# Optimization experiments

Measured on AMD Instinct MI355X. Metric: run time of the kernel, lower is better.

## Reference

```python
import jax, jax.numpy as jnp
import numpy as np


def _block_triu_mask(seq_len, rows_per_block, cols_per_block, dtype=jnp.float32):
    # Block upper-triangular mask: block (i, j) is ones iff j >= i.
    tri = jnp.triu(jnp.ones((seq_len, seq_len), dtype=dtype))
    return jnp.kron(tri, jnp.ones((rows_per_block, cols_per_block), dtype=dtype))


def setup_inputs() -> dict:
    key = jax.random.key(0)
    k_x, k_w1, k_w2 = jax.random.split(key, 3)
    seq_len, input_dim, hidden_dim, output_dim = 64, 64, 128, 64
    batch = 256
    x = jax.random.normal(k_x, (batch, seq_len, input_dim), dtype=jnp.float32)
    # kaiming_uniform_(a=sqrt(5)) on [fan_in, fan_out] tensor -> bound = 1/sqrt(fan_in)
    fan1 = seq_len * input_dim
    W1 = jax.random.uniform(k_w1, (seq_len * input_dim, seq_len * hidden_dim),
                            minval=-1.0, maxval=1.0, dtype=jnp.float32) / np.sqrt(fan1)
    b1 = jnp.zeros((seq_len * hidden_dim,), dtype=jnp.float32)
    fan2 = seq_len * hidden_dim
    W2 = jax.random.uniform(k_w2, (seq_len * hidden_dim, seq_len * output_dim),
                            minval=-1.0, maxval=1.0, dtype=jnp.float32) / np.sqrt(fan2)
    b2 = jnp.zeros((seq_len * output_dim,), dtype=jnp.float32)
    return {"x": x, "W1": W1, "b1": b1, "W2": W2, "b2": b2, "seq_len": seq_len}


def reference(x, W1, b1, W2, b2, seq_len):
    batch = x.shape[0]
    input_dim = x.shape[2]
    hidden_dim = W1.shape[1] // seq_len
    output_dim = W2.shape[1] // seq_len
    mask1 = _block_triu_mask(seq_len, input_dim, hidden_dim, W1.dtype)
    mask2 = _block_triu_mask(seq_len, hidden_dim, output_dim, W2.dtype)
    h = x.reshape(batch, seq_len * input_dim)
    h = jnp.matmul(h, W1 * mask1) + b1           # [B, S*H]
    h = jax.nn.relu(h)
    h = jnp.matmul(h, W2 * mask2) + b2           # [B, S*O]
    return h.reshape(batch, seq_len, output_dim)
```

## Files before the change

kernel.cpp:

```cpp
#include <hip/hip_runtime.h>

typedef short bf16x8 __attribute__((ext_vector_type(8)));
typedef float f32x4 __attribute__((ext_vector_type(4)));

__device__ __forceinline__ unsigned short f2bf(float f) {
  unsigned x = __float_as_uint(f);
  return (unsigned short)((x + 0x7fffu + ((x >> 16) & 1u)) >> 16);
}

__global__ __launch_bounds__(256)
void init_bias(const float* __restrict__ b, float* __restrict__ out) {
  int i = (blockIdx.x * 256 + threadIdx.x) * 4;
  *(float4*)(out + i) = *(const float4*)(b + (i & 4095));
}

__global__ __launch_bounds__(256)
void bias_relu_inplace(float* __restrict__ h, const float* __restrict__ b) {
  int i = (blockIdx.x * 256 + threadIdx.x) * 4;
  float4 v = *(const float4*)(h + i);
  float4 bv = *(const float4*)(b + (i & 8191));
  v.x = fmaxf(v.x + bv.x, 0.f);
  v.y = fmaxf(v.y + bv.y, 0.f);
  v.z = fmaxf(v.z + bv.z, 0.f);
  v.w = fmaxf(v.w + bv.w, 0.f);
  *(float4*)(h + i) = v;
}

template<int KROW, int CW, int KS>
__global__ __launch_bounds__(256, 3)
void gemm_sk(const float* __restrict__ A, const float* __restrict__ W,
             float* __restrict__ out, int K, int N)
{
  __shared__ unsigned short Xs[128 * 72];
  __shared__ unsigned short Ws[64 * 72];

  const int n0 = blockIdx.x * 64;
  const int m0 = blockIdx.y * 128;
  const int nIter = ((n0 / CW) + 1) * (KROW / 64);
  const int i0 = ((int)blockIdx.z) * nIter / KS;
  const int i1 = ((int)blockIdx.z + 1) * nIter / KS;
  if (i0 == i1) return;
  const int kbeg = i0 * 64, kend = i1 * 64;

  const int tid  = threadIdx.x;
  const int lane = tid & 63, wave = tid >> 6;
  const int l15  = lane & 15, quad = lane >> 4;
  const int wm0  = (wave & 1) * 64, wn0 = (wave >> 1) * 32;

  const int cg = tid & 7;
  const int rw = tid >> 3;

  float4 av[4][2];
  float4 wv[2][2];

  auto loadG = [&](int kt) {
    const float* ap = A + (size_t)(m0 + rw) * K + kt + cg * 8;
#pragma unroll
    for (int i = 0; i < 4; ++i) {
      av[i][0] = *(const float4*)(ap + (size_t)i * 32 * K);
      av[i][1] = *(const float4*)(ap + (size_t)i * 32 * K + 4);
    }
#pragma unroll
    for (int i = 0; i < 2; ++i) {
      const float* wp = W + (size_t)(kt + i * 32 + rw) * N + n0 + cg * 8;
      wv[i][0] = *(const float4*)wp;
      wv[i][1] = *(const float4*)(wp + 4);
    }
  };

  auto storeLDS = [&]() {
#pragma unroll
    for (int i = 0; i < 4; ++i) {
      union { unsigned short u[8]; int4 v; } t;
      const float* f = (const float*)&av[i][0];
#pragma unroll
      for (int j = 0; j < 8; ++j) t.u[j] = f2bf(f[j]);
      *(int4*)(&Xs[(rw + i * 32) * 72 + cg * 8]) = t.v;
    }
#pragma unroll
    for (int i = 0; i < 2; ++i) {
      const int r = i * 32 + rw;
      const float* f = (const float*)&wv[i][0];
#pragma unroll
      for (int j = 0; j < 8; ++j)
        Ws[(cg * 8 + j) * 72 + (r ^ (cg << 3))] = f2bf(f[j]);
    }
  };

  f32x4 acc[4][2];
#pragma unroll
  for (int mi = 0; mi < 4; ++mi)
#pragma unroll
    for (int ni = 0; ni < 2; ++ni)
      acc[mi][ni] = (f32x4){0.f, 0.f, 0.f, 0.f};

  loadG(kbeg);
  for (int kt = kbeg; kt < kend; kt += 64) {
    __syncthreads();
    storeLDS();
    if (kt + 64 < kend) loadG(kt + 64);
    __syncthreads();
#pragma unroll
    for (int kk = 0; kk < 64; kk += 32) {
      bf16x8 af[4], bf[2];
#pragma unroll
      for (int mi = 0; mi < 4; ++mi)
        af[mi] = *(const bf16x8*)(&Xs[(wm0 + mi * 16 + l15) * 72 + kk + quad * 8]);
#pragma unroll
      for (int ni = 0; ni < 2; ++ni) {
        const int n_l = wn0 + ni * 16 + l15;
        bf[ni] = *(const bf16x8*)(&Ws[n_l * 72 + ((kk + quad * 8) ^ ((n_l >> 3) << 3))]);
      }
#pragma unroll
      for (int mi = 0; mi < 4; ++mi)
#pragma unroll
        for (int ni = 0; ni < 2; ++ni)
          acc[mi][ni] = __builtin_amdgcn_mfma_f32_16x16x32_bf16(
              af[mi], bf[ni], acc[mi][ni], 0, 0, 0);
    }
  }

#pragma unroll
  for (int mi = 0; mi < 4; ++mi) {
#pragma unroll
    for (int ni = 0; ni < 2; ++ni) {
      const int n_out = n0 + wn0 + ni * 16 + l15;
#pragma unroll
      for (int r = 0; r < 4; ++r) {
        const int m_out = m0 + wm0 + mi * 16 + quad * 4 + r;
        atomicAdd(&out[(size_t)m_out * N + n_out], acc[mi][ni][r]);
      }
    }
  }
}

extern "C" void kernel_launch(void* const* d_in, const int* in_sizes, int n_in,
                              void* d_out, int out_size, void* d_ws, size_t ws_size,
                              hipStream_t stream) {
  const float* x  = (const float*)d_in[0];
  const float* W1 = (const float*)d_in[1];
  const float* b1 = (const float*)d_in[2];
  const float* W2 = (const float*)d_in[3];
  const float* b2 = (const float*)d_in[4];

  float* H_acc = (float*)d_ws;
  float* out   = (float*)d_out;

  hipMemsetAsync(H_acc, 0, (size_t)256 * 8192 * sizeof(float), stream);
  init_bias<<<dim3(1024), 256, 0, stream>>>(b2, out);

  gemm_sk<64, 128, 4><<<dim3(128, 2, 4), 256, 0, stream>>>(
      x, W1, H_acc, 4096, 8192);

  bias_relu_inplace<<<dim3(2048), 256, 0, stream>>>(H_acc, b1);

  gemm_sk<128, 64, 8><<<dim3(64, 2, 8), 256, 0, stream>>>(
      H_acc, W2, out, 8192, 4096);
}
```

Baseline: 329.8 us.

## Replace split-K atomics with partial buffers and fused reduce, bf16 hidden activations

```diff
diff --git a/kernel.cpp b/kernel.cpp
--- a/kernel.cpp
+++ b/kernel.cpp
@@ -9,40 +9,57 @@
 }
 
 __global__ __launch_bounds__(256)
-void init_bias(const float* __restrict__ b, float* __restrict__ out) {
-  int i = (blockIdx.x * 256 + threadIdx.x) * 4;
-  *(float4*)(out + i) = *(const float4*)(b + (i & 4095));
+void reduce1_relu_bf16(const float* __restrict__ hp, const float* __restrict__ b1,
+                       unsigned short* __restrict__ hbf) {
+  const size_t i = ((size_t)blockIdx.x * 256 + threadIdx.x) * 4;
+  f32x4 a = *(const f32x4*)(hp + i);
+#pragma unroll
+  for (int z = 1; z < 4; ++z)
+    a += *(const f32x4*)(hp + (size_t)z * 2097152 + i);
+  a += *(const f32x4*)(b1 + (i & 8191));
+  union { unsigned short u[4]; int2 v; } t;
+#pragma unroll
+  for (int j = 0; j < 4; ++j) t.u[j] = f2bf(fmaxf(a[j], 0.f));
+  *(int2*)(hbf + i) = t.v;
 }
 
 __global__ __launch_bounds__(256)
-void bias_relu_inplace(float* __restrict__ h, const float* __restrict__ b) {
-  int i = (blockIdx.x * 256 + threadIdx.x) * 4;
-  float4 v = *(const float4*)(h + i);
-  float4 bv = *(const float4*)(b + (i & 8191));
-  v.x = fmaxf(v.x + bv.x, 0.f);
-  v.y = fmaxf(v.y + bv.y, 0.f);
-  v.z = fmaxf(v.z + bv.z, 0.f);
-  v.w = fmaxf(v.w + bv.w, 0.f);
-  *(float4*)(h + i) = v;
+void reduce2_bias(const float* __restrict__ op, const float* __restrict__ b2,
+                  float* __restrict__ out) {
+  const size_t i = ((size_t)blockIdx.x * 256 + threadIdx.x) * 4;
+  f32x4 a = *(const f32x4*)(op + i);
+#pragma unroll
+  for (int z = 1; z < 8; ++z)
+    a += *(const f32x4*)(op + (size_t)z * 1048576 + i);
+  a += *(const f32x4*)(b2 + (i & 4095));
+  *(f32x4*)(out + i) = a;
 }
 
-template<int KROW, int CW, int KS>
+template<int KROW, int CW, int KS, bool ABF16>
 __global__ __launch_bounds__(256, 3)
-void gemm_sk(const float* __restrict__ A, const float* __restrict__ W,
-             float* __restrict__ out, int K, int N)
+void gemm_sk(const void* __restrict__ Av, const float* __restrict__ W,
+             float* __restrict__ part, int K, int N)
 {
   __shared__ unsigned short Xs[128 * 72];
   __shared__ unsigned short Ws[64 * 72];
 
-  const int n0 = blockIdx.x * 64;
+  const int xr = (int)gridDim.x - 1 - (int)blockIdx.x;
+  const int n0 = xr * 64;
   const int m0 = blockIdx.y * 128;
   const int nIter = ((n0 / CW) + 1) * (KROW / 64);
   const int i0 = ((int)blockIdx.z) * nIter / KS;
   const int i1 = ((int)blockIdx.z + 1) * nIter / KS;
-  if (i0 == i1) return;
+
+  float* po = part + (size_t)blockIdx.z * 256 * (size_t)N;
+  const int tid = threadIdx.x;
+
+  if (i0 == i1) {
+    for (int e = tid; e < 128 * 64; e += 256)
+      po[(size_t)(m0 + (e >> 6)) * N + n0 + (e & 63)] = 0.f;
+    return;
+  }
   const int kbeg = i0 * 64, kend = i1 * 64;
 
-  const int tid  = threadIdx.x;
   const int lane = tid & 63, wave = tid >> 6;
   const int l15  = lane & 15, quad = lane >> 4;
   const int wm0  = (wave & 1) * 64, wn0 = (wave >> 1) * 32;
@@ -51,14 +68,23 @@
   const int rw = tid >> 3;
 
   float4 av[4][2];
+  int4   ab[4];
   float4 wv[2][2];
 
   auto loadG = [&](int kt) {
-    const float* ap = A + (size_t)(m0 + rw) * K + kt + cg * 8;
+    if constexpr (ABF16) {
+      const unsigned short* ap =
+          (const unsigned short*)Av + (size_t)(m0 + rw) * K + kt + cg * 8;
 #pragma unroll
-    for (int i = 0; i < 4; ++i) {
-      av[i][0] = *(const float4*)(ap + (size_t)i * 32 * K);
-      av[i][1] = *(const float4*)(ap + (size_t)i * 32 * K + 4);
+      for (int i = 0; i < 4; ++i)
+        ab[i] = *(const int4*)(ap + (size_t)i * 32 * K);
+    } else {
+      const float* ap = (const float*)Av + (size_t)(m0 + rw) * K + kt + cg * 8;
+#pragma unroll
+      for (int i = 0; i < 4; ++i) {
+        av[i][0] = *(const float4*)(ap + (size_t)i * 32 * K);
+        av[i][1] = *(const float4*)(ap + (size_t)i * 32 * K + 4);
+      }
     }
 #pragma unroll
     for (int i = 0; i < 2; ++i) {
@@ -69,13 +95,19 @@
   };
 
   auto storeLDS = [&]() {
+    if constexpr (ABF16) {
 #pragma unroll
-    for (int i = 0; i < 4; ++i) {
-      union { unsigned short u[8]; int4 v; } t;
-      const float* f = (const float*)&av[i][0];
+      for (int i = 0; i < 4; ++i)
+        *(int4*)(&Xs[(rw + i * 32) * 72 + cg * 8]) = ab[i];
+    } else {
 #pragma unroll
-      for (int j = 0; j < 8; ++j) t.u[j] = f2bf(f[j]);
-      *(int4*)(&Xs[(rw + i * 32) * 72 + cg * 8]) = t.v;
+      for (int i = 0; i < 4; ++i) {
+        union { unsigned short u[8]; int4 v; } t;
+        const float* f = (const float*)&av[i][0];
+#pragma unroll
+        for (int j = 0; j < 8; ++j) t.u[j] = f2bf(f[j]);
+        *(int4*)(&Xs[(rw + i * 32) * 72 + cg * 8]) = t.v;
+      }
     }
 #pragma unroll
     for (int i = 0; i < 2; ++i) {
@@ -128,7 +160,7 @@
 #pragma unroll
       for (int r = 0; r < 4; ++r) {
         const int m_out = m0 + wm0 + mi * 16 + quad * 4 + r;
-        atomicAdd(&out[(size_t)m_out * N + n_out], acc[mi][ni][r]);
+        po[(size_t)m_out * N + n_out] = acc[mi][ni][r];
       }
     }
   }
@@ -143,17 +175,18 @@
   const float* W2 = (const float*)d_in[3];
   const float* b2 = (const float*)d_in[4];
 
-  float* H_acc = (float*)d_ws;
-  float* out   = (float*)d_out;
+  float* Hp = (float*)d_ws;
+  unsigned short* Hbf = (unsigned short*)(Hp + (size_t)4 * 2097152);
+  float* Op = (float*)(Hbf + 2097152);
+  float* out = (float*)d_out;
 
-  hipMemsetAsync(H_acc, 0, (size_t)256 * 8192 * sizeof(float), stream);
-  init_bias<<<dim3(1024), 256, 0, stream>>>(b2, out);
+  gemm_sk<64, 128, 4, false><<<dim3(128, 2, 4), 256, 0, stream>>>(
+      x, W1, Hp, 4096, 8192);
 
-  gemm_sk<64, 128, 4><<<dim3(128, 2, 4), 256, 0, stream>>>(
-      x, W1, H_acc, 4096, 8192);
+  reduce1_relu_bf16<<<dim3(2048), 256, 0, stream>>>(Hp, b1, Hbf);
 
-  bias_relu_inplace<<<dim3(2048), 256, 0, stream>>>(H_acc, b1);
+  gemm_sk<128, 64, 8, true><<<dim3(64, 2, 8), 256, 0, stream>>>(
+      Hbf, W2, Op, 8192, 4096);
 
-  gemm_sk<128, 64, 8><<<dim3(64, 2, 8), 256, 0, stream>>>(
-      H_acc, W2, out, 8192, 4096);
+  reduce2_bias<<<dim3(1024), 256, 0, stream>>>(Op, b2, out);
 }
```

Measured after the change: 377.0 us. 1.14x slower.

## Pre-pack inputs and weights into bf16 LDS-ready tile images for GEMMs

Applied to the files above, without the earlier changes.

```diff
diff --git a/kernel.cpp b/kernel.cpp
--- a/kernel.cpp
+++ b/kernel.cpp
@@ -8,6 +8,76 @@
   return (unsigned short)((x + 0x7fffu + ((x >> 16) & 1u)) >> 16);
 }
 
+
+__global__ __launch_bounds__(256)
+void pack_x(const float* __restrict__ x, unsigned short* __restrict__ img) {
+  const int i = (blockIdx.x * 256 + threadIdx.x) * 8;
+  const int m = i >> 12, k = i & 4095;
+  float q[8];
+  *(float4*)(q)     = *(const float4*)(x + i);
+  *(float4*)(q + 4) = *(const float4*)(x + i + 4);
+  union { unsigned short u[8]; int4 v; } t;
+#pragma unroll
+  for (int j = 0; j < 8; ++j) t.u[j] = f2bf(q[j]);
+  const size_t o = (size_t)((m >> 7) * 64 + (k >> 6)) * 9216 + (m & 127) * 72 + (k & 63);
+  *(int4*)(img + o) = t.v;
+}
+
+__global__ __launch_bounds__(256)
+void pack_w1(const float* __restrict__ W, unsigned short* __restrict__ img) {
+  const int p = blockIdx.x;
+  const int kt = blockIdx.y;
+  if (kt > p) return;
+  __shared__ unsigned short S[9216];
+  const int r  = threadIdx.x >> 2;
+  const int c0 = (threadIdx.x & 3) * 32;
+  const float* src = W + (size_t)(kt * 64 + r) * 8192 + p * 128 + c0;
+  float q[32];
+#pragma unroll
+  for (int j = 0; j < 8; ++j) *(float4*)(q + j * 4) = *(const float4*)(src + j * 4);
+#pragma unroll
+  for (int j = 0; j < 32; ++j) {
+    const int n = c0 + j;
+    S[n * 72 + (r ^ (((n >> 3) & 7) << 3))] = f2bf(q[j]);
+  }
+  __syncthreads();
+  unsigned short* dst = img + (size_t)(p * (p + 1) / 2 + kt) * 9216;
+#pragma unroll
+  for (int i = 0; i < 9; ++i) {
+    const int s = (threadIdx.x + i * 256) * 4;
+    *(int2*)(dst + s) = *(const int2*)(S + s);
+  }
+}
+
+__global__ __launch_bounds__(256)
+void pack_w2(const float* __restrict__ W, unsigned short* __restrict__ img) {
+  const int p = blockIdx.x;
+  const int kt = blockIdx.y;
+  if (kt >= 4 * p + 4) return;
+  __shared__ unsigned short S[9216];
+  const int r  = threadIdx.x >> 2;
+  const int c0 = (threadIdx.x & 3) * 32;
+  const int k  = kt * 64 + r;
+  const int lk = (2 * p + 1 + (c0 >= 64 ? 1 : 0)) * 128;
+  const float* src = W + (size_t)k * 4096 + p * 128 + c0;
+  float q[32];
+#pragma unroll
+  for (int j = 0; j < 8; ++j) *(float4*)(q + j * 4) = *(const float4*)(src + j * 4);
+  const float sc = (k < lk) ? 1.f : 0.f;
+#pragma unroll
+  for (int j = 0; j < 32; ++j) {
+    const int n = c0 + j;
+    S[n * 72 + (r ^ (((n >> 3) & 7) << 3))] = f2bf(q[j] * sc);
+  }
+  __syncthreads();
+  unsigned short* dst = img + (size_t)(2 * p * (p + 1) + kt) * 9216;
+#pragma unroll
+  for (int i = 0; i < 9; ++i) {
+    const int s = (threadIdx.x + i * 256) * 4;
+    *(int2*)(dst + s) = *(const int2*)(S + s);
+  }
+}
+
 __global__ __launch_bounds__(256)
 void init_bias(const float* __restrict__ b, float* __restrict__ out) {
   int i = (blockIdx.x * 256 + threadIdx.x) * 4;
@@ -15,115 +85,98 @@
 }
 
 __global__ __launch_bounds__(256)
-void bias_relu_inplace(float* __restrict__ h, const float* __restrict__ b) {
-  int i = (blockIdx.x * 256 + threadIdx.x) * 4;
-  float4 v = *(const float4*)(h + i);
-  float4 bv = *(const float4*)(b + (i & 8191));
-  v.x = fmaxf(v.x + bv.x, 0.f);
-  v.y = fmaxf(v.y + bv.y, 0.f);
-  v.z = fmaxf(v.z + bv.z, 0.f);
-  v.w = fmaxf(v.w + bv.w, 0.f);
-  *(float4*)(h + i) = v;
-}
-
-template<int KROW, int CW, int KS>
+void bias_relu_pack(const float* __restrict__ h, const float* __restrict__ b1,
+                    unsigned short* __restrict__ img) {
+  const int i = (blockIdx.x * 256 + threadIdx.x) * 8;
+  const int m = i >> 13, k = i & 8191;
+  float q[8];
+  *(float4*)(q)     = *(const float4*)(h + i);
+  *(float4*)(q + 4) = *(const float4*)(h + i + 4);
+  union { unsigned short u[8]; int4 v; } t;
+#pragma unroll
+  for (int j = 0; j < 8; ++j)
+    t.u[j] = f2bf(fmaxf(q[j] + b1[k + j], 0.f));
+  const size_t o = (size_t)((m >> 7) * 128 + (k >> 6)) * 9216 + (m & 127) * 72 + (k & 63);
+  *(int4*)(img + o) = t.v;
+}
+
+template<int IM, int IA, int KT, int KS>
 __global__ __launch_bounds__(256, 3)
-void gemm_sk(const float* __restrict__ A, const float* __restrict__ W,
-             float* __restrict__ out, int K, int N)
-{
-  __shared__ unsigned short Xs[128 * 72];
-  __shared__ unsigned short Ws[64 * 72];
-
-  const int n0 = blockIdx.x * 64;
-  const int m0 = blockIdx.y * 128;
-  const int nIter = ((n0 / CW) + 1) * (KROW / 64);
-  const int i0 = ((int)blockIdx.z) * nIter / KS;
+void gemm_img(const unsigned short* __restrict__ Aimg,
+              const unsigned short* __restrict__ Wimg,
+              float* __restrict__ out, int N) {
+  __shared__ unsigned short Xs[9216];
+  __shared__ unsigned short Ws[9216];
+
+  const int p  = (int)gridDim.x - 1 - (int)blockIdx.x;
+  const int mt = blockIdx.y;
+  const int nIter = p * IM + IA;
+  const int i0 = (int)blockIdx.z * nIter / KS;
   const int i1 = ((int)blockIdx.z + 1) * nIter / KS;
   if (i0 == i1) return;
-  const int kbeg = i0 * 64, kend = i1 * 64;
-
-  const int tid  = threadIdx.x;
-  const int lane = tid & 63, wave = tid >> 6;
-  const int l15  = lane & 15, quad = lane >> 4;
-  const int wm0  = (wave & 1) * 64, wn0 = (wave >> 1) * 32;
-
-  const int cg = tid & 7;
-  const int rw = tid >> 3;
-
-  float4 av[4][2];
-  float4 wv[2][2];
-
+
+  const size_t tb = (size_t)IM * ((size_t)p * (p - 1) / 2) + (size_t)IA * p;
+  const char* Wp = (const char*)Wimg + tb * 18432;
+  const char* Ap = (const char*)Aimg + (size_t)mt * KT * 18432;
+
+  const int tid = threadIdx.x, lane = tid & 63, wave = tid >> 6;
+  const int l15 = lane & 15, quad = lane >> 4;
+  const int wm0 = (wave & 1) * 64, wn0 = (wave >> 1) * 64;
+
+  const char* gsrc0 = (wave < 2) ? Ap : Wp;
+  const int   half  = (wave & 1) * 9216;
+  char*       ldst  = ((wave < 2) ? (char*)Xs : (char*)Ws) + half;
+  const int   loff  = lane * 16;
+
+  int4 st[9];
   auto loadG = [&](int kt) {
-    const float* ap = A + (size_t)(m0 + rw) * K + kt + cg * 8;
-#pragma unroll
-    for (int i = 0; i < 4; ++i) {
-      av[i][0] = *(const float4*)(ap + (size_t)i * 32 * K);
-      av[i][1] = *(const float4*)(ap + (size_t)i * 32 * K + 4);
-    }
-#pragma unroll
-    for (int i = 0; i < 2; ++i) {
-      const float* wp = W + (size_t)(kt + i * 32 + rw) * N + n0 + cg * 8;
-      wv[i][0] = *(const float4*)wp;
-      wv[i][1] = *(const float4*)(wp + 4);
-    }
+    const char* g = gsrc0 + (size_t)kt * 18432 + half + loff;
+#pragma unroll
+    for (int j = 0; j < 9; ++j) st[j] = *(const int4*)(g + j * 1024);
   };
-
-  auto storeLDS = [&]() {
-#pragma unroll
-    for (int i = 0; i < 4; ++i) {
-      union { unsigned short u[8]; int4 v; } t;
-      const float* f = (const float*)&av[i][0];
-#pragma unroll
-      for (int j = 0; j < 8; ++j) t.u[j] = f2bf(f[j]);
-      *(int4*)(&Xs[(rw + i * 32) * 72 + cg * 8]) = t.v;
-    }
-#pragma unroll
-    for (int i = 0; i < 2; ++i) {
-      const int r = i * 32 + rw;
-      const float* f = (const float*)&wv[i][0];
-#pragma unroll
-      for (int j = 0; j < 8; ++j)
-        Ws[(cg * 8 + j) * 72 + (r ^ (cg << 3))] = f2bf(f[j]);
-    }
+  auto storeL = [&]() {
+#pragma unroll
+    for (int j = 0; j < 9; ++j) *(int4*)(ldst + loff + j * 1024) = st[j];
   };
 
-  f32x4 acc[4][2];
+  f32x4 acc[4][4];
 #pragma unroll
   for (int mi = 0; mi < 4; ++mi)
 #pragma unroll
-    for (int ni = 0; ni < 2; ++ni)
+    for (int ni = 0; ni < 4; ++ni)
       acc[mi][ni] = (f32x4){0.f, 0.f, 0.f, 0.f};
 
-  loadG(kbeg);
-  for (int kt = kbeg; kt < kend; kt += 64) {
+  loadG(i0);
+  for (int kt = i0; kt < i1; ++kt) {
     __syncthreads();
-    storeLDS();
-    if (kt + 64 < kend) loadG(kt + 64);
+    storeL();
+    if (kt + 1 < i1) loadG(kt + 1);
     __syncthreads();
 #pragma unroll
     for (int kk = 0; kk < 64; kk += 32) {
-      bf16x8 af[4], bf[2];
+      bf16x8 af[4], bfr[4];
 #pragma unroll
       for (int mi = 0; mi < 4; ++mi)
         af[mi] = *(const bf16x8*)(&Xs[(wm0 + mi * 16 + l15) * 72 + kk + quad * 8]);
 #pragma unroll
-      for (int ni = 0; ni < 2; ++ni) {
-        const int n_l = wn0 + ni * 16 + l15;
-        bf[ni] = *(const bf16x8*)(&Ws[n_l * 72 + ((kk + quad * 8) ^ ((n_l >> 3) << 3))]);
+      for (int ni = 0; ni < 4; ++ni) {
+        const int n = wn0 + ni * 16 + l15;
+        bfr[ni] = *(const bf16x8*)(&Ws[n * 72 + ((kk + quad * 8) ^ (((n >> 3) & 7) << 3))]);
       }
 #pragma unroll
       for (int mi = 0; mi < 4; ++mi)
 #pragma unroll
-        for (int ni = 0; ni < 2; ++ni)
+        for (int ni = 0; ni < 4; ++ni)
           acc[mi][ni] = __builtin_amdgcn_mfma_f32_16x16x32_bf16(
-              af[mi], bf[ni], acc[mi][ni], 0, 0, 0);
+              af[mi], bfr[ni], acc[mi][ni], 0, 0, 0);
     }
   }
 
-#pragma unroll
-  for (int mi = 0; mi < 4; ++mi) {
-#pragma unroll
-    for (int ni = 0; ni < 2; ++ni) {
+  const int m0 = mt * 128, n0 = p * 128;
+#pragma unroll
+  for (int mi = 0; mi < 4; ++mi)
+#pragma unroll
+    for (int ni = 0; ni < 4; ++ni) {
       const int n_out = n0 + wn0 + ni * 16 + l15;
 #pragma unroll
       for (int r = 0; r < 4; ++r) {
@@ -131,7 +184,6 @@
         atomicAdd(&out[(size_t)m_out * N + n_out], acc[mi][ni][r]);
       }
     }
-  }
 }
 
 extern "C" void kernel_launch(void* const* d_in, const int* in_sizes, int n_in,
@@ -143,17 +195,25 @@
   const float* W2 = (const float*)d_in[3];
   const float* b2 = (const float*)d_in[4];
 
-  float* H_acc = (float*)d_ws;
-  float* out   = (float*)d_out;
-
+  char* ws = (char*)d_ws;
+  unsigned short* Ximg  = (unsigned short*)ws;
+  unsigned short* W1img = (unsigned short*)(ws + 2359296);
+  unsigned short* Himg  = (unsigned short*)(ws + 2359296 + 38338560);
+  unsigned short* W2img = (unsigned short*)(ws + 2359296 + 38338560 + 4718592);
+  float*          H_acc = (float*)(ws + 2359296 + 38338560 + 4718592 + 38928384);
+  float* out = (float*)d_out;
+
+  pack_x <<<dim3(512),      256, 0, stream>>>(x,  Ximg);
+  pack_w1<<<dim3(64, 64),   256, 0, stream>>>(W1, W1img);
+  pack_w2<<<dim3(32, 128),  256, 0, stream>>>(W2, W2img);
   hipMemsetAsync(H_acc, 0, (size_t)256 * 8192 * sizeof(float), stream);
-  init_bias<<<dim3(1024), 256, 0, stream>>>(b2, out);
-
-  gemm_sk<64, 128, 4><<<dim3(128, 2, 4), 256, 0, stream>>>(
-      x, W1, H_acc, 4096, 8192);
-
-  bias_relu_inplace<<<dim3(2048), 256, 0, stream>>>(H_acc, b1);
-
-  gemm_sk<128, 64, 8><<<dim3(64, 2, 8), 256, 0, stream>>>(
-      H_acc, W2, out, 8192, 4096);
-}
+  init_bias<<<dim3(1024),   256, 0, stream>>>(b2, out);
+
+  gemm_img<1, 1, 64, 8><<<dim3(64, 2, 8), 256, 0, stream>>>(
+      Ximg, W1img, H_acc, 8192);
+
+  bias_relu_pack<<<dim3(1024), 256, 0, stream>>>(H_acc, b1, Himg);
+
+  gemm_img<4, 4, 128, 16><<<dim3(32, 2, 16), 256, 0, stream>>>(
+      Himg, W2img, out, 4096);
+}
```

Measured after the change: 469.7 us. 42.4% more time.

## Pre-pack activations to bf16 swizzled image and replace atomics with partial-sum reduction

Applied to the files above, without the earlier changes.

```diff
diff --git a/kernel.cpp b/kernel.cpp
--- a/kernel.cpp
+++ b/kernel.cpp
@@ -8,130 +8,182 @@
   return (unsigned short)((x + 0x7fffu + ((x >> 16) & 1u)) >> 16);
 }
 
+
+__device__ __forceinline__ int chunkbase1(int p) {
+  const int a = p >> 1, b = p & 1;
+  const int al = a >> 3, be = a & 7;
+  const int C8 = 4 * al * (al + 1) + be * (al + 1);
+  return 2 * C8 + b * ((a + 8) >> 3);
+}
+__device__ __forceinline__ int chunkbase2(int p) {
+  const int al = p >> 2, be = p & 3;
+  return 2 * al * (al + 1) + be * (al + 1);
+}
+
 __global__ __launch_bounds__(256)
-void init_bias(const float* __restrict__ b, float* __restrict__ out) {
-  int i = (blockIdx.x * 256 + threadIdx.x) * 4;
-  *(float4*)(out + i) = *(const float4*)(b + (i & 4095));
-}
-
-__global__ __launch_bounds__(256)
-void bias_relu_inplace(float* __restrict__ h, const float* __restrict__ b) {
-  int i = (blockIdx.x * 256 + threadIdx.x) * 4;
-  float4 v = *(const float4*)(h + i);
-  float4 bv = *(const float4*)(b + (i & 8191));
-  v.x = fmaxf(v.x + bv.x, 0.f);
-  v.y = fmaxf(v.y + bv.y, 0.f);
-  v.z = fmaxf(v.z + bv.z, 0.f);
-  v.w = fmaxf(v.w + bv.w, 0.f);
-  *(float4*)(h + i) = v;
-}
-
-template<int KROW, int CW, int KS>
-__global__ __launch_bounds__(256, 3)
-void gemm_sk(const float* __restrict__ A, const float* __restrict__ W,
-             float* __restrict__ out, int K, int N)
-{
-  __shared__ unsigned short Xs[128 * 72];
+void pack_x(const float* __restrict__ x, unsigned short* __restrict__ img) {
+  const int i = (blockIdx.x * 256 + threadIdx.x) * 8;
+  const int m = i >> 12, k = i & 4095;
+  float q[8];
+  *(float4*)(q)     = *(const float4*)(x + i);
+  *(float4*)(q + 4) = *(const float4*)(x + i + 4);
+  union { unsigned short u[8]; int4 v; } t;
+#pragma unroll
+  for (int j = 0; j < 8; ++j) t.u[j] = f2bf(q[j]);
+  const size_t o = (size_t)(k >> 6) * 16384 + m * 64 + ((k & 63) ^ ((m & 7) << 3));
+  *(int4*)(img + o) = t.v;
+}
+
+template<int PSH, int KSH, int MODE>
+__global__ __launch_bounds__(256, 2)
+void gemm_sk(const unsigned short* __restrict__ Aimg,
+             const float* __restrict__ W,
+             float* __restrict__ part, int N) {
   __shared__ unsigned short Ws[64 * 72];
 
-  const int n0 = blockIdx.x * 64;
-  const int m0 = blockIdx.y * 128;
-  const int nIter = ((n0 / CW) + 1) * (KROW / 64);
-  const int i0 = ((int)blockIdx.z) * nIter / KS;
-  const int i1 = ((int)blockIdx.z + 1) * nIter / KS;
-  if (i0 == i1) return;
-  const int kbeg = i0 * 64, kend = i1 * 64;
-
-  const int tid  = threadIdx.x;
-  const int lane = tid & 63, wave = tid >> 6;
-  const int l15  = lane & 15, quad = lane >> 4;
-  const int wm0  = (wave & 1) * 64, wn0 = (wave >> 1) * 32;
-
-  const int cg = tid & 7;
-  const int rw = tid >> 3;
-
-  float4 av[4][2];
-  float4 wv[2][2];
-
-  auto loadG = [&](int kt) {
-    const float* ap = A + (size_t)(m0 + rw) * K + kt + cg * 8;
-#pragma unroll
-    for (int i = 0; i < 4; ++i) {
-      av[i][0] = *(const float4*)(ap + (size_t)i * 32 * K);
-      av[i][1] = *(const float4*)(ap + (size_t)i * 32 * K + 4);
-    }
-#pragma unroll
-    for (int i = 0; i < 2; ++i) {
-      const float* wp = W + (size_t)(kt + i * 32 + rw) * N + n0 + cg * 8;
-      wv[i][0] = *(const float4*)wp;
-      wv[i][1] = *(const float4*)(wp + 4);
-    }
-  };
-
-  auto storeLDS = [&]() {
-#pragma unroll
-    for (int i = 0; i < 4; ++i) {
-      union { unsigned short u[8]; int4 v; } t;
-      const float* f = (const float*)&av[i][0];
-#pragma unroll
-      for (int j = 0; j < 8; ++j) t.u[j] = f2bf(f[j]);
-      *(int4*)(&Xs[(rw + i * 32) * 72 + cg * 8]) = t.v;
-    }
-#pragma unroll
-    for (int i = 0; i < 2; ++i) {
-      const int r = i * 32 + rw;
-      const float* f = (const float*)&wv[i][0];
-#pragma unroll
-      for (int j = 0; j < 8; ++j)
-        Ws[(cg * 8 + j) * 72 + (r ^ (cg << 3))] = f2bf(f[j]);
-    }
-  };
-
-  f32x4 acc[4][2];
-#pragma unroll
-  for (int mi = 0; mi < 4; ++mi)
-#pragma unroll
-    for (int ni = 0; ni < 2; ++ni)
-      acc[mi][ni] = (f32x4){0.f, 0.f, 0.f, 0.f};
-
-  loadG(kbeg);
-  for (int kt = kbeg; kt < kend; kt += 64) {
-    __syncthreads();
-    storeLDS();
-    if (kt + 64 < kend) loadG(kt + 64);
-    __syncthreads();
-#pragma unroll
-    for (int kk = 0; kk < 64; kk += 32) {
-      bf16x8 af[4], bf[2];
-#pragma unroll
-      for (int mi = 0; mi < 4; ++mi)
-        af[mi] = *(const bf16x8*)(&Xs[(wm0 + mi * 16 + l15) * 72 + kk + quad * 8]);
-#pragma unroll
-      for (int ni = 0; ni < 2; ++ni) {
-        const int n_l = wn0 + ni * 16 + l15;
-        bf[ni] = *(const bf16x8*)(&Ws[n_l * 72 + ((kk + quad * 8) ^ ((n_l >> 3) << 3))]);
-      }
-#pragma unroll
-      for (int mi = 0; mi < 4; ++mi)
-#pragma unroll
-        for (int ni = 0; ni < 2; ++ni)
-          acc[mi][ni] = __builtin_amdgcn_mfma_f32_16x16x32_bf16(
-              af[mi], bf[ni], acc[mi][ni], 0, 0, 0);
+  const int p = (int)gridDim.x - 1 - (int)blockIdx.x;
+  const int c = blockIdx.y;
+  const int nt = ((p >> PSH) + 1) << KSH;
+  const int i0 = c * 8;
+  if (i0 >= nt) return;
+  const int i1 = (i0 + 8 < nt) ? i0 + 8 : nt;
+  const int base = (MODE == 1) ? chunkbase1(p) : chunkbase2(p);
+  float* po = part + (size_t)(base + c) * 16384;
+
+  const int tid = threadIdx.x, lane = tid & 63, wave = tid >> 6;
+  const int l15 = lane & 15, quad = lane >> 4;
+
+  const int l16 = tid & 15, rg = tid >> 4;
+  const float* wbase = W + (size_t)p * 64 + l16 * 4;
+
+  int aoff[4][2];
+#pragma unroll
+  for (int mi = 0; mi < 4; ++mi) {
+    const int m = wave * 64 + mi * 16 + l15;
+#pragma unroll
+    for (int h = 0; h < 2; ++h) {
+      const int k8 = h * 32 + quad * 8;
+      aoff[mi][h] = m * 64 + (k8 ^ ((m & 7) << 3));
     }
   }
 
-#pragma unroll
-  for (int mi = 0; mi < 4; ++mi) {
-#pragma unroll
-    for (int ni = 0; ni < 2; ++ni) {
-      const int n_out = n0 + wn0 + ni * 16 + l15;
-#pragma unroll
-      for (int r = 0; r < 4; ++r) {
-        const int m_out = m0 + wm0 + mi * 16 + quad * 4 + r;
-        atomicAdd(&out[(size_t)m_out * N + n_out], acc[mi][ni][r]);
+  float4 wr[4];
+  bf16x8 afA[4][2], afB[4][2];
+
+  auto loadW = [&](int kt) {
+#pragma unroll
+    for (int j = 0; j < 4; ++j)
+      wr[j] = *(const float4*)(wbase + (size_t)(kt * 64 + rg + j * 16) * N);
+  };
+  auto loadA = [&](bf16x8 (&af)[4][2], int kt) {
+    const unsigned short* at = Aimg + (size_t)kt * 16384;
+#pragma unroll
+    for (int mi = 0; mi < 4; ++mi)
+#pragma unroll
+      for (int h = 0; h < 2; ++h)
+        af[mi][h] = *(const bf16x8*)(at + aoff[mi][h]);
+  };
+  auto storeW = [&]() {
+#pragma unroll
+    for (int j = 0; j < 4; ++j) {
+      const int r = rg + j * 16;
+      const float* f = (const float*)&wr[j];
+#pragma unroll
+      for (int i = 0; i < 4; ++i) {
+        const int cc = l16 * 4 + i;
+        Ws[cc * 72 + (r ^ (((cc >> 3) & 7) << 3))] = f2bf(f[i]);
       }
     }
+  };
+
+  f32x4 acc[4][4];
+#pragma unroll
+  for (int mi = 0; mi < 4; ++mi)
+#pragma unroll
+    for (int ni = 0; ni < 4; ++ni)
+      acc[mi][ni] = (f32x4){0.f, 0.f, 0.f, 0.f};
+
+  auto STEP = [&](bf16x8 (&cur)[4][2], bf16x8 (&nxt)[4][2], int it) {
+    __syncthreads();
+    storeW();
+    if (it + 1 < i1) { loadW(it + 1); loadA(nxt, it + 1); }
+    __syncthreads();
+#pragma unroll
+    for (int h = 0; h < 2; ++h) {
+      const int kk = h * 32;
+      bf16x8 bfr[4];
+#pragma unroll
+      for (int ni = 0; ni < 4; ++ni) {
+        const int n = ni * 16 + l15;
+        bfr[ni] = *(const bf16x8*)(
+            &Ws[n * 72 + ((kk + quad * 8) ^ (((n >> 3) & 7) << 3))]);
+      }
+#pragma unroll
+      for (int mi = 0; mi < 4; ++mi)
+#pragma unroll
+        for (int ni = 0; ni < 4; ++ni)
+          acc[mi][ni] = __builtin_amdgcn_mfma_f32_16x16x32_bf16(
+              cur[mi][h], bfr[ni], acc[mi][ni], 0, 0, 0);
+    }
+  };
+
+  loadW(i0);
+  loadA(afA, i0);
+  int it = i0;
+  while (true) {
+    STEP(afA, afB, it); if (++it >= i1) break;
+    STEP(afB, afA, it); if (++it >= i1) break;
   }
+
+  float* ps = po + wave * 4096 + lane;
+#pragma unroll
+  for (int mi = 0; mi < 4; ++mi)
+#pragma unroll
+    for (int ni = 0; ni < 4; ++ni)
+#pragma unroll
+      for (int r = 0; r < 4; ++r)
+        ps[mi * 1024 + ni * 256 + r * 64] = acc[mi][ni][r];
+}
+
+__global__ __launch_bounds__(256)
+void reduce1(const float* __restrict__ P, const float* __restrict__ b1,
+             unsigned short* __restrict__ img) {
+  const int g = blockIdx.x * 256 + threadIdx.x;
+  const int p = g >> 12;
+  const int s = (g & 4095) * 4;
+  const int nc = ((p >> 1) + 8) >> 3;
+  const float* ps = P + (size_t)chunkbase1(p) * 16384 + s;
+  f32x4 a = *(const f32x4*)ps;
+  for (int ci = 1; ci < nc; ++ci)
+    a += *(const f32x4*)(ps + (size_t)ci * 16384);
+  const int lane = s & 63, r = (s >> 6) & 3, ni = (s >> 8) & 3;
+  const int mi = (s >> 10) & 3, wv = (s >> 12) & 3;
+  const int m  = wv * 64 + mi * 16 + (lane >> 4) * 4 + r;
+  const int nl = ni * 16 + (lane & 15);
+  a += *(const f32x4*)(b1 + p * 64 + nl);
+  union { unsigned short u[4]; int2 v; } t;
+#pragma unroll
+  for (int j = 0; j < 4; ++j) t.u[j] = f2bf(fmaxf(a[j], 0.f));
+  *(int2*)(img + (size_t)p * 16384 + m * 64 + (nl ^ ((m & 7) << 3))) = t.v;
+}
+
+__global__ __launch_bounds__(256)
+void reduce2(const float* __restrict__ P, const float* __restrict__ b2,
+             float* __restrict__ out) {
+  const int g = blockIdx.x * 256 + threadIdx.x;
+  const int p = g >> 12;
+  const int s = (g & 4095) * 4;
+  const int nc = (p + 4) >> 2;
+  const float* ps = P + (size_t)chunkbase2(p) * 16384 + s;
+  f32x4 a = *(const f32x4*)ps;
+  for (int ci = 1; ci < nc; ++ci)
+    a += *(const f32x4*)(ps + (size_t)ci * 16384);
+  const int lane = s & 63, r = (s >> 6) & 3, ni = (s >> 8) & 3;
+  const int mi = (s >> 10) & 3, wv = (s >> 12) & 3;
+  const int m  = wv * 64 + mi * 16 + (lane >> 4) * 4 + r;
+  const int nl = ni * 16 + (lane & 15);
+  a += *(const f32x4*)(b2 + p * 64 + nl);
+  *(f32x4*)(out + (size_t)m * 4096 + p * 64 + nl) = a;
 }
 
 extern "C" void kernel_launch(void* const* d_in, const int* in_sizes, int n_in,
@@ -143,17 +195,19 @@
   const float* W2 = (const float*)d_in[3];
   const float* b2 = (const float*)d_in[4];
 
-  float* H_acc = (float*)d_ws;
-  float* out   = (float*)d_out;
-
-  hipMemsetAsync(H_acc, 0, (size_t)256 * 8192 * sizeof(float), stream);
-  init_bias<<<dim3(1024), 256, 0, stream>>>(b2, out);
-
-  gemm_sk<64, 128, 4><<<dim3(128, 2, 4), 256, 0, stream>>>(
-      x, W1, H_acc, 4096, 8192);
-
-  bias_relu_inplace<<<dim3(2048), 256, 0, stream>>>(H_acc, b1);
-
-  gemm_sk<128, 64, 8><<<dim3(64, 2, 8), 256, 0, stream>>>(
-      H_acc, W2, out, 8192, 4096);
-}
+  char* ws = (char*)d_ws;
+  unsigned short* Ximg = (unsigned short*)ws;
+  unsigned short* Himg = (unsigned short*)(ws + 2097152);
+  float*          P    = (float*)(ws + 6291456);
+  float* out = (float*)d_out;
+
+  pack_x<<<dim3(512), 256, 0, stream>>>(x, Ximg);
+
+  gemm_sk<1, 0, 1><<<dim3(128, 8), 256, 0, stream>>>(Ximg, W1, P, 8192);
+
+  reduce1<<<dim3(2048), 256, 0, stream>>>(P, b1, Himg);
+
+  gemm_sk<0, 1, 2><<<dim3(64, 16), 256, 0, stream>>>(Himg, W2, P, 4096);
+
+  reduce2<<<dim3(1024), 256, 0, stream>>>(P, b2, out);
+}
```

Result: slower. 338.5 us (+2.7%).
